# Kernel tuning notes

Hardware: AMD Instinct MI355X
Metric: run time of the kernel (lower is better)

The kernel has to match this reference:

```python
import jax, jax.numpy as jnp
import numpy as np

N = 50000      # nodes
E = 800000     # edges
H = 128        # hidden_features
EF = 8         # edge_features (before distance concat)
L = 2          # num_layers
NF = 100.0     # normalization_factor
NC = 1.0       # norm_constant
ATTN = True
USE_TANH = False
TANH_RANGE = 15.0
EIN = 2 * H + EF + 1  # GCL / coord-MLP edge input dim


def setup_inputs() -> dict:
    key = jax.random.key(0)
    ks = jax.random.split(key, 16)
    s = 0.02
    w = lambda k, shape: (jax.random.normal(k, shape, jnp.float32) * s)
    return dict(
        x=jax.random.normal(ks[0], (N, H), jnp.float32),
        pos=jax.random.normal(ks[1], (N, 3), jnp.float32),
        mask=jnp.ones((N, 1), jnp.float32),
        edge_attr=jax.random.normal(ks[2], (E, EF), jnp.float32),
        edge_index=jax.random.randint(ks[3], (2, E), 0, N),
        # GCL layer params, stacked over L layers
        W_e1=w(ks[4], (L, EIN, H)), b_e1=jnp.zeros((L, H), jnp.float32),
        W_e2=w(ks[5], (L, H, H)),  b_e2=jnp.zeros((L, H), jnp.float32),
        W_att=w(ks[6], (L, H, 1)), b_att=jnp.zeros((L, 1), jnp.float32),
        W_n1=w(ks[7], (L, 2 * H, H)), b_n1=jnp.zeros((L, H), jnp.float32),
        W_n2=w(ks[8], (L, H, H)),  b_n2=jnp.zeros((L, H), jnp.float32),
        # Equivariant coordinate-update MLP (last layer has no bias)
        cW1=w(ks[9], (EIN, H)), cb1=jnp.zeros((H,), jnp.float32),
        cW2=w(ks[10], (H, H)), cb2=jnp.zeros((H,), jnp.float32),
        cW3=w(ks[11], (H, 1)),
    )


def reference(x, pos, mask, edge_attr, edge_index,
              W_e1, b_e1, W_e2, b_e2, W_att, b_att, W_n1, b_n1, W_n2, b_n2,
              cW1, cb1, cW2, cb2, cW3):
    silu = jax.nn.silu
    row, col = edge_index[0], edge_index[1]  # aggregate messages at row
    diff = pos[row] - pos[col]                         # [E, 3]
    d2 = jnp.sum(diff * diff, axis=-1, keepdims=True)  # [E, 1] squared distance
    ea = jnp.concatenate([d2, edge_attr], axis=-1)     # [E, EF+1]

    # GCL message-passing layers (residual node update)
    for l in range(L):
        he = jnp.concatenate([x[row], x[col], ea], axis=-1)   # [E, EIN]
        m = silu(silu(he @ W_e1[l] + b_e1[l]) @ W_e2[l] + b_e2[l])
        if ATTN:
            m = m * jax.nn.sigmoid(m @ W_att[l] + b_att[l])
        agg = jax.ops.segment_sum(m, row, num_segments=N) / NF
        x = x + silu(jnp.concatenate([x, agg], axis=-1) @ W_n1[l] + b_n1[l]) @ W_n2[l] + b_n2[l]

    # Equivariant coordinate update
    he = jnp.concatenate([x[row], x[col], ea], axis=-1)
    phi = silu(silu(he @ cW1 + cb1) @ cW2 + cb2) @ cW3        # [E, 1]
    if USE_TANH:
        phi = jnp.tanh(phi) * TANH_RANGE
    nd = diff / (jnp.sqrt(d2) + NC)                           # normalized direction
    trans = nd * phi                                          # [E, 3]
    pos = pos + (jax.ops.segment_sum(trans, row, num_segments=N) / NF) * mask
    return (x, pos)
```

## Files before the change

### kernel.cpp

```cpp
#include <hip/hip_runtime.h>
#include <hip/hip_bf16.h>
#include <stdint.h>

#define NN 50000
#define NE 800000
#define HH 128

typedef __bf16 bf16x8 __attribute__((ext_vector_type(8)));
typedef float  f32x4  __attribute__((ext_vector_type(4)));
typedef long   f8frag;

__device__ __forceinline__ unsigned short f2bf(float f) {
  union { float f; uint32_t u; } v; v.f = f;
  uint32_t r = v.u + 0x7FFFu + ((v.u >> 16) & 1u);
  return (unsigned short)(r >> 16);
}
__device__ __forceinline__ float b2f(unsigned short u) {
  union { float f; uint32_t u; } v; v.u = (uint32_t)u << 16; return v.f;
}
#if __has_builtin(__builtin_amdgcn_cvt_pk_bf16_f32)
typedef __bf16 bf16x2 __attribute__((ext_vector_type(2)));
__device__ __forceinline__ uint32_t pack2bf(float a, float b) {
  union { bf16x2 v; uint32_t u; } t;
  t.v = __builtin_amdgcn_cvt_pk_bf16_f32(a, b);
  return t.u;
}
#else
__device__ __forceinline__ uint32_t pack2bf(float a, float b) {
  return (uint32_t)f2bf(a) | ((uint32_t)f2bf(b) << 16);
}
#endif
__device__ __forceinline__ uint8_t f2fp8(float v) {
  return (uint8_t)(__builtin_amdgcn_cvt_pk_fp8_f32(v, 0.f, 0, false) & 0xff);
}
__device__ __forceinline__ float silu_f(float x) {
  return x * __builtin_amdgcn_rcpf(1.f + __expf(-x));
}
__device__ __forceinline__ float sigm_f(float x) {
  return __builtin_amdgcn_rcpf(1.f + __expf(-x));
}

__device__ __forceinline__ bf16x8 frag_ld(const short* blk, int row, int q) {
  int c = q ^ ((row >> 1) & 3);
  return *(const bf16x8*)(blk + row * 32 + c * 8);
}
__device__ __forceinline__ int wfrag_off(int row, int q) {
  return row * 32 + ((q ^ ((row >> 1) & 3)) * 8);
}

__global__ void k_prep_weights(const float* We1, const float* We2, const float* Wn1,
                               const float* Wn2, const float* cW1, const float* cW2,
                               uint8_t* W1f8, short* W2sw, short* Wn1sw, short* Wn2sw,
                               short* W1csw) {
  int idx = blockIdx.x * 256 + threadIdx.x;
  if (idx < 110592) {
    int l = idx / 36864, rem = idx % 36864;
    const float* s = (l == 0) ? We1 : (l == 1) ? We1 + 33920 : cW1;
    int kkb = rem >> 12, r2 = rem & 4095;
    int n = r2 >> 5, kw = r2 & 31;
    int k = kkb * 32 + kw;
    float v = (k < 265) ? s[k * 128 + n] : 0.f;
    W1f8[idx] = f2fp8(v);
    return;
  }
  idx -= 110592;
  if (idx < 49152) {
    int l = idx >> 14, rem = idx & 16383;
    const float* s = (l == 0) ? We2 : (l == 1) ? We2 + 16384 : cW2;
    int kkb = rem >> 12, r2 = rem & 4095, n = r2 >> 5, kw = r2 & 31;
    int cp = kw >> 3, j = kw & 7, c = cp ^ ((n >> 1) & 3);
    int k = kkb * 32 + c * 8 + j;
    W2sw[(l << 14) + (rem)] = (short)f2bf(s[k * 128 + n]);
    return;
  }
  idx -= 49152;
  if (idx < 65536) {
    int l = idx >> 15, rem = idx & 32767;
    const float* s = Wn1 + l * 32768;
    int kkb = rem >> 12, r2 = rem & 4095, n = r2 >> 5, kw = r2 & 31;
    int cp = kw >> 3, j = kw & 7, c = cp ^ ((n >> 1) & 3);
    int k = kkb * 32 + c * 8 + j;
    Wn1sw[(l << 15) + rem] = (short)f2bf(s[k * 128 + n]);
    return;
  }
  idx -= 65536;
  if (idx < 32768) {
    int l = idx >> 14, rem = idx & 16383;
    const float* s = Wn2 + l * 16384;
    int kkb = rem >> 12, r2 = rem & 4095, n = r2 >> 5, kw = r2 & 31;
    int cp = kw >> 3, j = kw & 7, c = cp ^ ((n >> 1) & 3);
    int k = kkb * 32 + c * 8 + j;
    Wn2sw[(l << 14) + rem] = (short)f2bf(s[k * 128 + n]);
    return;
  }
  idx -= 32768;
  if (idx < 98304) {
    int l = idx / 32768, rem = idx % 32768;
    const float* s = (l == 0) ? We1 : (l == 1) ? We1 + 33920 : cW1;
    int kkb = rem >> 13, r2 = rem & 8191, n = r2 >> 5, kw = r2 & 31;
    int cp = kw >> 3, j = kw & 7, c = cp ^ ((n >> 1) & 3);
    int k = kkb * 32 + c * 8 + j;
    float v = (n < 128) ? s[k * 128 + n] : s[(128 + k) * 128 + (n - 128)];
    W1csw[l * 32768 + rem] = (short)f2bf(v);
  }
}

__global__ void k_x_prep(const float* __restrict__ x, short* __restrict__ Anode) {
  int i = blockIdx.x * 256 + threadIdx.x;
  if (i < NN * 32) {
    float4 v = ((const float4*)x)[i];
    ushort4 pk;
    pk.x = f2bf(v.x); pk.y = f2bf(v.y); pk.z = f2bf(v.z); pk.w = f2bf(v.w);
    *(ushort4*)(Anode + i * 4) = pk;
  }
}
__global__ void k_edge_pre(const float* __restrict__ pos, const float* __restrict__ eattr,
                           const int* __restrict__ ei, const int* __restrict__ inv,
                           int* __restrict__ rowS, int* __restrict__ colS,
                           uint8_t* __restrict__ eaF8, float* __restrict__ ndS) {
  int e = blockIdx.x * 256 + threadIdx.x;
  if (e >= NE) return;
  int r = ei[e], c = ei[NE + e];
  float dx = pos[r * 3 + 0] - pos[c * 3 + 0];
  float dy = pos[r * 3 + 1] - pos[c * 3 + 1];
  float dz = pos[r * 3 + 2] - pos[c * 3 + 2];
  float d2 = dx * dx + dy * dy + dz * dz;
  float invd = __builtin_amdgcn_rcpf(sqrtf(d2) + 1.f);
  int p = inv[e];
  rowS[p] = r;
  colS[p] = c;
  ndS[p * 3 + 0] = dx * invd;
  ndS[p * 3 + 1] = dy * invd;
  ndS[p * 3 + 2] = dz * invd;
  const float* ea = eattr + (size_t)e * 8;
  uint32_t w0 = __builtin_amdgcn_cvt_pk_fp8_f32(d2, ea[0], 0, false);
  w0 = __builtin_amdgcn_cvt_pk_fp8_f32(ea[1], ea[2], w0, true);
  uint32_t w1 = __builtin_amdgcn_cvt_pk_fp8_f32(ea[3], ea[4], 0, false);
  w1 = __builtin_amdgcn_cvt_pk_fp8_f32(ea[5], ea[6], w1, true);
  uint32_t w2 = __builtin_amdgcn_cvt_pk_fp8_f32(ea[7], 0.f, 0, false);
  uint4 v = {w0, w1, w2, 0u};
  *(uint4*)(eaF8 + (size_t)p * 16) = v;
}
__global__ void k_pos_final(const float* __restrict__ pos, const float* __restrict__ mask,
                            const float* __restrict__ pagg, float* __restrict__ out) {
  int i = blockIdx.x * 256 + threadIdx.x;
  if (i < NN * 3) out[i] = pos[i] + pagg[i] * 0.01f * mask[i / 3];
}

__global__ void k_hist(const int* __restrict__ ei, int* __restrict__ cnt) {
  int e = blockIdx.x * 256 + threadIdx.x;
  if (e < NE) atomicAdd(&cnt[ei[e]], 1);
}
__global__ void k_scan_block(const int* __restrict__ cnt, int* __restrict__ offs,
                             int* __restrict__ bsum) {
  __shared__ int s[256];
  int i = blockIdx.x * 256 + threadIdx.x;
  int v = (i < NN) ? cnt[i] : 0;
  s[threadIdx.x] = v;
  __syncthreads();
#pragma unroll
  for (int d = 1; d < 256; d <<= 1) {
    int t = (threadIdx.x >= d) ? s[threadIdx.x - d] : 0;
    __syncthreads();
    s[threadIdx.x] += t;
    __syncthreads();
  }
  if (i < NN) offs[i] = s[threadIdx.x] - v;
  if (threadIdx.x == 255) bsum[blockIdx.x] = s[255];
}
__global__ void k_scan_top(int* __restrict__ bsum) {
  __shared__ int s[256];
  int v = (threadIdx.x < 196) ? bsum[threadIdx.x] : 0;
  s[threadIdx.x] = v;
  __syncthreads();
#pragma unroll
  for (int d = 1; d < 256; d <<= 1) {
    int t = (threadIdx.x >= d) ? s[threadIdx.x - d] : 0;
    __syncthreads();
    s[threadIdx.x] += t;
    __syncthreads();
  }
  if (threadIdx.x < 196) bsum[threadIdx.x] = s[threadIdx.x] - v;
}
__global__ void k_scan_add(int* __restrict__ offs, const int* __restrict__ bsum) {
  int i = blockIdx.x * 256 + threadIdx.x;
  if (i < NN) offs[i] += bsum[blockIdx.x];
}
__global__ void k_scatter(const int* __restrict__ ei, int* __restrict__ offs,
                          int* __restrict__ inv) {
  int e = blockIdx.x * 256 + threadIdx.x;
  if (e < NE) inv[e] = atomicAdd(&offs[ei[e]], 1);
}

__global__ __launch_bounds__(256) void k_h1(
    const short* __restrict__ Anode, const short* __restrict__ W1c,
    const float* __restrict__ b1, short* __restrict__ H1RC) {
  const int tid = threadIdx.x, lane = tid & 63, w = tid >> 6;
  const int ln = lane & 15, q = lane >> 4;
  const int tile = blockIdx.x;
  size_t nbase[4];
  int wofs[4];
#pragma unroll
  for (int i = 0; i < 4; ++i) {
    int node = tile * 64 + i * 16 + ln;
    nbase[i] = (size_t)(node < NN ? node : (NN - 1)) * 128;
    int row = w * 64 + i * 16 + ln;
    wofs[i] = row * 32 + ((q ^ ((row >> 1) & 3)) * 8);
  }
  f32x4 acc[4][4];
  const f32x4 zero4 = {0.f, 0.f, 0.f, 0.f};
#pragma unroll
  for (int mi = 0; mi < 4; ++mi)
#pragma unroll
    for (int ni = 0; ni < 4; ++ni) acc[mi][ni] = zero4;
#pragma unroll
  for (int kk = 0; kk < 4; ++kk) {
    bf16x8 af[4], bfr[4];
#pragma unroll
    for (int i = 0; i < 4; ++i) af[i] = *(const bf16x8*)(Anode + nbase[i] + kk * 32 + q * 8);
#pragma unroll
    for (int i = 0; i < 4; ++i) bfr[i] = *(const bf16x8*)(W1c + kk * 8192 + wofs[i]);
#pragma unroll
    for (int mi = 0; mi < 4; ++mi)
#pragma unroll
      for (int ni = 0; ni < 4; ++ni)
        acc[mi][ni] = __builtin_amdgcn_mfma_f32_16x16x32_bf16(af[mi], bfr[ni], acc[mi][ni], 0, 0, 0);
  }
  float b1v[4];
#pragma unroll
  for (int ni = 0; ni < 4; ++ni) {
    int ch = w * 64 + ni * 16 + ln;
    b1v[ni] = (ch < 128) ? b1[ch] : 0.f;
  }
#pragma unroll
  for (int mi = 0; mi < 4; ++mi)
#pragma unroll
    for (int r = 0; r < 4; ++r) {
      int node = tile * 64 + mi * 16 + q * 4 + r;
      if (node < NN) {
#pragma unroll
        for (int ni = 0; ni < 4; ++ni) {
          int ph = (w >> 1) * 128 + (w & 1) * 64 + ((ln >> 2) << 4) + (ni << 2) + (ln & 3);
          H1RC[(size_t)node * 256 + ph] = (short)f2bf(acc[mi][ni][r] + b1v[ni]);
        }
      }
    }
}

template <int COORD>
__global__ __launch_bounds__(256, 4) void k_edge_gemm(
    const short* __restrict__ H1RC, const uint8_t* __restrict__ eaF8,
    const int* __restrict__ rowS, const int* __restrict__ colS,
    const uint8_t* __restrict__ W1f8, const short* __restrict__ W2l,
    const float* __restrict__ b2,
    const float* __restrict__ wred, const float* __restrict__ batt,
    const float* __restrict__ ndS, float* outAcc) {
  __shared__ __align__(16) short A2s[8192];
  __shared__ float redp[64][2];
  __shared__ __align__(16) unsigned short attb[64];
  __shared__ int srow[64];
  __shared__ __align__(8) unsigned char srunS[64];
  __shared__ int runrowS[64];
  __shared__ int cntS[1];

  const int tid = threadIdx.x;
  const int lane = tid & 63;
  const int w = tid >> 6;
  const int ln = lane & 15, q = lane >> 4;
  const int wm = w >> 1, wn = w & 1;
  const int tile = blockIdx.x;

  if (tid < 64) srow[tid] = rowS[tile * 64 + tid];
  __syncthreads();

  bool is_start = (tid < 64) && (tid == 0 || srow[tid] != srow[tid - 1]);
  unsigned long long bmask = __ballot(is_start);
  if (tid == 0) cntS[0] = __popcll(bmask);
  if (tid < 64) {
    int run = __popcll(bmask & ((1ull << lane) - 1ull)) + (is_start ? 1 : 0) - 1;
    srunS[tid] = (unsigned char)run;
    if (is_start) runrowS[run] = srow[tid];
  }

  const int e0 = wm * 32 + ln, e1 = e0 + 16;
  const uint32_t cbp = (uint32_t)(wn * 64 + q * 16);
  const uint32_t hr0 = (uint32_t)srow[e0] * 256u + cbp;
  const uint32_t hr1 = (uint32_t)srow[e1] * 256u + cbp;
  const uint32_t hc0 = (uint32_t)colS[tile * 64 + e0] * 256u + 128u + cbp;
  const uint32_t hc1 = (uint32_t)colS[tile * 64 + e1] * 256u + 128u + cbp;
  const uint32_t ea0 = (uint32_t)(tile * 64 + e0) * 16u + (uint32_t)((q & 1) * 8);
  const uint32_t ea1 = (uint32_t)(tile * 64 + e1) * 16u + (uint32_t)((q & 1) * 8);
  int wofs8[4], wofs[4];
#pragma unroll
  for (int i = 0; i < 4; ++i) {
    wofs8[i] = (wn * 64 + i * 16 + ln) * 32 + q * 8;
    wofs[i] = wfrag_off(wn * 64 + i * 16 + ln, q);
  }

  union U8 { uint4 v; unsigned short s[8]; };
  U8 xr[2][2], xc[2][2];
  xr[0][0].v = *(const uint4*)(H1RC + hr0);
  xr[0][1].v = *(const uint4*)(H1RC + hr0 + 8);
  xr[1][0].v = *(const uint4*)(H1RC + hr1);
  xr[1][1].v = *(const uint4*)(H1RC + hr1 + 8);
  xc[0][0].v = *(const uint4*)(H1RC + hc0);
  xc[0][1].v = *(const uint4*)(H1RC + hc0 + 8);
  xc[1][0].v = *(const uint4*)(H1RC + hc1);
  xc[1][1].v = *(const uint4*)(H1RC + hc1 + 8);

  f32x4 acc[4][2];
  const f32x4 zero4 = {0.f, 0.f, 0.f, 0.f};
#pragma unroll
  for (int ni = 0; ni < 4; ++ni)
#pragma unroll
    for (int mi = 0; mi < 2; ++mi) acc[ni][mi] = zero4;

  {
    const uint8_t* W1ea = W1f8 + 8 * 4096;
    f8frag wf[4], hf[2];
#pragma unroll
    for (int i = 0; i < 4; ++i) wf[i] = *(const f8frag*)(W1ea + wofs8[i]);
    hf[0] = (q < 2) ? *(const f8frag*)(eaF8 + ea0) : 0L;
    hf[1] = (q < 2) ? *(const f8frag*)(eaF8 + ea1) : 0L;
#pragma unroll
    for (int ni = 0; ni < 4; ++ni)
#pragma unroll
      for (int mi = 0; mi < 2; ++mi)
        acc[ni][mi] = __builtin_amdgcn_mfma_f32_16x16x32_fp8_fp8(wf[ni], hf[mi], acc[ni][mi], 0, 0, 0);
  }

#pragma unroll
  for (int ni = 0; ni < 4; ++ni) {
    int cb = wn * 64 + ni * 16 + q * 4;
    int kkb = cb >> 5, cc = (cb >> 3) & 3, j0 = cb & 7;
    const int hh = ni >> 1, b4 = (ni & 1) * 4;
#pragma unroll
    for (int mi = 0; mi < 2; ++mi) {
      int edge = wm * 32 + mi * 16 + ln;
      int addr = kkb * 2048 + edge * 32 + ((cc ^ ((edge >> 1) & 3)) * 8) + j0;
      float h0 = silu_f(acc[ni][mi][0] + b2f(xr[mi][hh].s[b4 + 0]) + b2f(xc[mi][hh].s[b4 + 0]));
      float h1 = silu_f(acc[ni][mi][1] + b2f(xr[mi][hh].s[b4 + 1]) + b2f(xc[mi][hh].s[b4 + 1]));
      float h2 = silu_f(acc[ni][mi][2] + b2f(xr[mi][hh].s[b4 + 2]) + b2f(xc[mi][hh].s[b4 + 2]));
      float h3 = silu_f(acc[ni][mi][3] + b2f(xr[mi][hh].s[b4 + 3]) + b2f(xc[mi][hh].s[b4 + 3]));
      uint2 pk;
      pk.x = pack2bf(h0, h1);
      pk.y = pack2bf(h2, h3);
      *(uint2*)(A2s + addr) = pk;
    }
  }
  __syncthreads();

  f32x4 acc2[4][2];
#pragma unroll
  for (int ni = 0; ni < 4; ++ni)
#pragma unroll
    for (int mi = 0; mi < 2; ++mi) acc2[ni][mi] = zero4;
#pragma unroll
  for (int kk = 0; kk < 4; ++kk) {
    bf16x8 wf[4], hf[2];
#pragma unroll
    for (int i = 0; i < 4; ++i) wf[i] = *(const bf16x8*)(W2l + kk * 4096 + wofs[i]);
#pragma unroll
    for (int i = 0; i < 2; ++i) hf[i] = frag_ld(A2s + kk * 2048, wm * 32 + i * 16 + ln, q);
#pragma unroll
    for (int ni = 0; ni < 4; ++ni)
#pragma unroll
      for (int mi = 0; mi < 2; ++mi)
        acc2[ni][mi] = __builtin_amdgcn_mfma_f32_16x16x32_bf16(wf[ni], hf[mi], acc2[ni][mi], 0, 0, 0);
  }

  float4 b2v[4], wv[4];
#pragma unroll
  for (int ni = 0; ni < 4; ++ni) {
    b2v[ni] = *(const float4*)(b2 + wn * 64 + ni * 16 + q * 4);
    wv[ni]  = *(const float4*)(wred + wn * 64 + ni * 16 + q * 4);
  }
  float p[2] = {0.f, 0.f};
#pragma unroll
  for (int ni = 0; ni < 4; ++ni)
#pragma unroll
    for (int mi = 0; mi < 2; ++mi)
#pragma unroll
      for (int r = 0; r < 4; ++r) {
        float v = silu_f(acc2[ni][mi][r] + ((const float*)&b2v[ni])[r]);
        acc2[ni][mi][r] = v;
        p[mi] += v * ((const float*)&wv[ni])[r];
      }
#pragma unroll
  for (int mi = 0; mi < 2; ++mi) {
    p[mi] += __shfl_xor(p[mi], 16, 64);
    p[mi] += __shfl_xor(p[mi], 32, 64);
  }
  if (lane < 16) {
#pragma unroll
    for (int mi = 0; mi < 2; ++mi) redp[wm * 32 + mi * 16 + ln][wn] = p[mi];
  }
  __syncthreads();

  if (COORD == 0) {
    if (tid < 64) attb[tid] = f2bf(sigm_f(redp[tid][0] + redp[tid][1] + batt[0]));
#pragma unroll
    for (int ni = 0; ni < 4; ++ni)
#pragma unroll
      for (int mi = 0; mi < 2; ++mi) {
        int eb = mi * 16 + ln;
        int cE = (eb >> 3) & 3, jE = eb & 7;
#pragma unroll
        for (int r = 0; r < 4; ++r) {
          int chan2 = wn * 64 + ni * 16 + q * 4 + r;
          int addr = wm * 4096 + chan2 * 32 + ((cE ^ ((chan2 >> 1) & 3)) * 8) + jE;
          union { float f; uint32_t u; } vv;
          vv.f = acc2[ni][mi][r];
          A2s[addr] = (short)((vv.u + 0x8000u) >> 16);
        }
      }
    __syncthreads();
    const int nruns = cntS[0];
    bf16x8 bfrg[2][2];
#pragma unroll
    for (int kk = 0; kk < 2; ++kk)
#pragma unroll
      for (int ni = 0; ni < 2; ++ni)
        bfrg[kk][ni] = frag_ld(A2s + kk * 4096, w * 32 + ni * 16 + ln, q);
    const int npass = (nruns + 15) >> 4;
    for (int pp = 0; pp < npass; ++pp) {
      const unsigned int base = pp * 16;
      f32x4 a3c[2] = {zero4, zero4};
#pragma unroll
      for (int kk = 0; kk < 2; ++kk) {
        uint2 sb = *(const uint2*)(srunS + kk * 32 + q * 8);
        U8 ab;
        ab.v = *(const uint4*)(attb + kk * 32 + q * 8);
        union { short s[8]; bf16x8 v; } af;
#pragma unroll
        for (int j = 0; j < 4; ++j)
          af.s[j] = (((sb.x >> (8 * j)) & 255u) == base + (unsigned)ln) ? (short)ab.s[j] : (short)0;
#pragma unroll
        for (int j = 0; j < 4; ++j)
          af.s[4 + j] = (((sb.y >> (8 * j)) & 255u) == base + (unsigned)ln) ? (short)ab.s[4 + j] : (short)0;
        a3c[0] = __builtin_amdgcn_mfma_f32_16x16x32_bf16(af.v, bfrg[kk][0], a3c[0], 0, 0, 0);
        a3c[1] = __builtin_amdgcn_mfma_f32_16x16x32_bf16(af.v, bfrg[kk][1], a3c[1], 0, 0, 0);
      }
#pragma unroll
      for (int ni = 0; ni < 2; ++ni)
#pragma unroll
        for (int r = 0; r < 4; ++r) {
          int run = (int)base + q * 4 + r;
          if (run < nruns) {
            int rw = runrowS[run];
            atomicAdd(&outAcc[(size_t)rw * 128 + (w * 32 + ni * 16 + ln)], a3c[ni][r]);
          }
        }
    }
  } else {
    float* ndl = (float*)A2s;
    if (tid < 64) {
      float phi = redp[tid][0] + redp[tid][1];
      ndl[tid * 3 + 0] = ndS[(size_t)(tile * 64 + tid) * 3 + 0] * phi;
      ndl[tid * 3 + 1] = ndS[(size_t)(tile * 64 + tid) * 3 + 1] * phi;
      ndl[tid * 3 + 2] = ndS[(size_t)(tile * 64 + tid) * 3 + 2] * phi;
    }
    __syncthreads();
    if (is_start) {
      int myrow = srow[tid];
      float s0 = 0.f, s1 = 0.f, s2 = 0.f;
      for (int j = tid; j < 64 && srow[j] == myrow; ++j) {
        s0 += ndl[j * 3 + 0];
        s1 += ndl[j * 3 + 1];
        s2 += ndl[j * 3 + 2];
      }
      atomicAdd(&outAcc[myrow * 3 + 0], s0);
      atomicAdd(&outAcc[myrow * 3 + 1], s1);
      atomicAdd(&outAcc[myrow * 3 + 2], s2);
    }
  }
}

__global__ __launch_bounds__(256) void k_node_gemm(
    short* Anode, const float* __restrict__ agg,
    const short* __restrict__ Wn1l, const short* __restrict__ Wn2l,
    const float* __restrict__ b1, const float* __restrict__ b2,
    const float* __restrict__ xres, float* __restrict__ xout) {
  __shared__ short A2s[4 * 2048];

  const int tid = threadIdx.x;
  const int lane = tid & 63;
  const int w = tid >> 6;
  const int ln = lane & 15, q = lane >> 4;
  const int wm = w >> 1, wn = w & 1;
  const int tile = blockIdx.x;

  int nidx[2];
  size_t nbase[2];
  int wofs[4];
#pragma unroll
  for (int i = 0; i < 2; ++i) {
    int node = tile * 64 + wm * 32 + i * 16 + ln;
    nidx[i] = node < NN ? node : (NN - 1);
    nbase[i] = (size_t)nidx[i] * 128;
  }
#pragma unroll
  for (int i = 0; i < 4; ++i) wofs[i] = wfrag_off(wn * 64 + i * 16 + ln, q);

  f32x4 acc[2][4];
  const f32x4 zero4 = {0.f, 0.f, 0.f, 0.f};
#pragma unroll
  for (int mi = 0; mi < 2; ++mi)
#pragma unroll
    for (int ni = 0; ni < 4; ++ni) acc[mi][ni] = zero4;

#pragma unroll
  for (int kk = 0; kk < 8; ++kk) {
    bf16x8 af[2], bfr[4];
#pragma unroll
    for (int i = 0; i < 2; ++i) {
      if (kk < 4) {
        af[i] = *(const bf16x8*)(Anode + nbase[i] + kk * 32 + q * 8);
      } else {
        const float* ag = agg + nbase[i] + (kk - 4) * 32 + q * 8;
        float4 lo = *(const float4*)ag;
        float4 hi = *(const float4*)(ag + 4);
        union { uint32_t u[4]; bf16x8 v; } t;
        t.u[0] = pack2bf(lo.x * 0.01f, lo.y * 0.01f);
        t.u[1] = pack2bf(lo.z * 0.01f, lo.w * 0.01f);
        t.u[2] = pack2bf(hi.x * 0.01f, hi.y * 0.01f);
        t.u[3] = pack2bf(hi.z * 0.01f, hi.w * 0.01f);
        af[i] = t.v;
      }
    }
#pragma unroll
    for (int i = 0; i < 4; ++i) bfr[i] = *(const bf16x8*)(Wn1l + kk * 4096 + wofs[i]);
#pragma unroll
    for (int mi = 0; mi < 2; ++mi)
#pragma unroll
      for (int ni = 0; ni < 4; ++ni)
        acc[mi][ni] = __builtin_amdgcn_mfma_f32_16x16x32_bf16(af[mi], bfr[ni], acc[mi][ni], 0, 0, 0);
  }

  float b1v[4];
#pragma unroll
  for (int ni = 0; ni < 4; ++ni) b1v[ni] = b1[wn * 64 + ni * 16 + ln];
#pragma unroll
  for (int mi = 0; mi < 2; ++mi)
#pragma unroll
    for (int ni = 0; ni < 4; ++ni) {
      int chan = wn * 64 + ni * 16 + ln;
      int kkb = chan >> 5, c = (chan >> 3) & 3, jj = chan & 7;
#pragma unroll
      for (int r = 0; r < 4; ++r) {
        int m = wm * 32 + mi * 16 + q * 4 + r;
        float v = silu_f(acc[mi][ni][r] + b1v[ni]);
        A2s[kkb * 2048 + m * 32 + ((c ^ ((m >> 1) & 3)) * 8) + jj] = (short)f2bf(v);
      }
    }
  __syncthreads();

  f32x4 acc2[2][4];
#pragma unroll
  for (int mi = 0; mi < 2; ++mi)
#pragma unroll
    for (int ni = 0; ni < 4; ++ni) acc2[mi][ni] = zero4;
#pragma unroll
  for (int kk = 0; kk < 4; ++kk) {
    bf16x8 af[2], bfr[4];
#pragma unroll
    for (int i = 0; i < 2; ++i) af[i] = frag_ld(A2s + kk * 2048, wm * 32 + i * 16 + ln, q);
#pragma unroll
    for (int i = 0; i < 4; ++i) bfr[i] = *(const bf16x8*)(Wn2l + kk * 4096 + wofs[i]);
#pragma unroll
    for (int mi = 0; mi < 2; ++mi)
#pragma unroll
      for (int ni = 0; ni < 4; ++ni)
        acc2[mi][ni] = __builtin_amdgcn_mfma_f32_16x16x32_bf16(af[mi], bfr[ni], acc2[mi][ni], 0, 0, 0);
  }

  float b2v[4];
#pragma unroll
  for (int ni = 0; ni < 4; ++ni) b2v[ni] = b2[wn * 64 + ni * 16 + ln];
#pragma unroll
  for (int mi = 0; mi < 2; ++mi)
#pragma unroll
    for (int r = 0; r < 4; ++r) {
      int m = wm * 32 + mi * 16 + q * 4 + r;
      int node = tile * 64 + m;
      if (node < NN) {
#pragma unroll
        for (int ni = 0; ni < 4; ++ni) {
          int chan = wn * 64 + ni * 16 + ln;
          float v = acc2[mi][ni][r] + b2v[ni] + xres[(size_t)node * 128 + chan];
          xout[(size_t)node * 128 + chan] = v;
          Anode[(size_t)node * 128 + chan] = (short)f2bf(v);
        }
      }
    }
}

extern "C" void kernel_launch(void* const* d_in, const int* in_sizes, int n_in,
                              void* d_out, int out_size, void* d_ws, size_t ws_size,
                              hipStream_t stream) {
  const float* x    = (const float*)d_in[0];
  const float* pos  = (const float*)d_in[1];
  const float* mask = (const float*)d_in[2];
  const float* eattr= (const float*)d_in[3];
  const int*   ei   = (const int*)d_in[4];
  const float* We1  = (const float*)d_in[5];
  const float* be1  = (const float*)d_in[6];
  const float* We2  = (const float*)d_in[7];
  const float* be2  = (const float*)d_in[8];
  const float* Watt = (const float*)d_in[9];
  const float* batt = (const float*)d_in[10];
  const float* Wn1  = (const float*)d_in[11];
  const float* bn1  = (const float*)d_in[12];
  const float* Wn2  = (const float*)d_in[13];
  const float* bn2  = (const float*)d_in[14];
  const float* cW1  = (const float*)d_in[15];
  const float* cb1  = (const float*)d_in[16];
  const float* cW2  = (const float*)d_in[17];
  const float* cb2  = (const float*)d_in[18];
  const float* cW3  = (const float*)d_in[19];

  char* p = (char*)d_ws;
  auto carve = [&](size_t bytes) { char* r = p; p += (bytes + 511) & ~(size_t)511; return r; };
  short*   Anode = (short*)carve((size_t)NN * 128 * 2);
  short*   H1RC  = (short*)carve((size_t)NN * 256 * 2);
  uint8_t* eaF8  = (uint8_t*)carve((size_t)NE * 16 + 256);
  int*     rowS  = (int*)carve((size_t)NE * 4);
  int*     colS  = (int*)carve((size_t)NE * 4);
  float*   ndS   = (float*)carve((size_t)NE * 3 * 4);
  float*   agg   = (float*)carve((size_t)NN * 128 * 4);
  float*   xcur  = (float*)carve((size_t)NN * 128 * 4);
  float*   pagg  = (float*)carve((size_t)NN * 3 * 4);
  uint8_t* W1f8  = (uint8_t*)carve(3 * 36864);
  short*   W2sw  = (short*)carve(3 * 16384 * 2);
  short*   Wn1sw = (short*)carve(2 * 32768 * 2);
  short*   Wn2sw = (short*)carve(2 * 16384 * 2);
  short*   W1csw = (short*)carve(3 * 32768 * 2);
  int*     cnt   = (int*)carve((size_t)NN * 4);
  int*     offs  = (int*)carve((size_t)NN * 4);
  int*     bsum  = (int*)carve(256 * 4);
  int*     inv   = (int*)carve((size_t)NE * 4);

  float* xout_f = (float*)d_out;
  float* pout_f = xout_f + NN * 128;

  k_prep_weights<<<1392, 256, 0, stream>>>(We1, We2, Wn1, Wn2, cW1, cW2,
                                           W1f8, W2sw, Wn1sw, Wn2sw, W1csw);
  k_x_prep<<<6250, 256, 0, stream>>>(x, Anode);

  hipMemsetAsync(cnt, 0, (size_t)NN * 4, stream);
  k_hist<<<3125, 256, 0, stream>>>(ei, cnt);
  k_scan_block<<<196, 256, 0, stream>>>(cnt, offs, bsum);
  k_scan_top<<<1, 256, 0, stream>>>(bsum);
  k_scan_add<<<196, 256, 0, stream>>>(offs, bsum);
  k_scatter<<<3125, 256, 0, stream>>>(ei, offs, inv);
  k_edge_pre<<<3125, 256, 0, stream>>>(pos, eattr, ei, inv, rowS, colS, eaF8, ndS);

  for (int l = 0; l < 2; ++l) {
    k_h1<<<782, 256, 0, stream>>>(Anode, W1csw + l * 32768, be1 + l * 128, H1RC);
    hipMemsetAsync(agg, 0, (size_t)NN * 128 * 4, stream);
    k_edge_gemm<0><<<12500, 256, 0, stream>>>(H1RC, eaF8, rowS, colS,
        W1f8 + l * 36864, W2sw + l * 16384, be2 + l * 128,
        Watt + l * 128, batt + l, (const float*)nullptr, agg);
    k_node_gemm<<<782, 256, 0, stream>>>(Anode, agg,
        Wn1sw + l * 32768, Wn2sw + l * 16384, bn1 + l * 128, bn2 + l * 128,
        l == 0 ? x : xcur, l == 0 ? xcur : xout_f);
  }
  k_h1<<<782, 256, 0, stream>>>(Anode, W1csw + 2 * 32768, cb1, H1RC);
  hipMemsetAsync(pagg, 0, (size_t)NN * 3 * 4, stream);
  k_edge_gemm<1><<<12500, 256, 0, stream>>>(H1RC, eaF8, rowS, colS,
      W1f8 + 2 * 36864, W2sw + 2 * 16384, cb2, cW3, (const float*)nullptr, ndS, pagg);
  k_pos_final<<<587, 256, 0, stream>>>(pos, mask, pagg, pout_f);
}
```

Before: 720.5 us.

## Fuse next-layer H1 projection into node GEMM and drop bf16 node copy

After: 712.2 us. No clear change (-1.2%).

```diff
diff --git a/kernel.cpp b/kernel.cpp
--- a/kernel.cpp
+++ b/kernel.cpp
@@ -46,6 +46,16 @@
 }
 __device__ __forceinline__ int wfrag_off(int row, int q) {
   return row * 32 + ((q ^ ((row >> 1) & 3)) * 8);
+}
+__device__ __forceinline__ bf16x8 fragf32(const float* src, float sc) {
+  float4 lo = *(const float4*)src;
+  float4 hi = *(const float4*)(src + 4);
+  union { uint32_t u[4]; bf16x8 v; } t;
+  t.u[0] = pack2bf(lo.x * sc, lo.y * sc);
+  t.u[1] = pack2bf(lo.z * sc, lo.w * sc);
+  t.u[2] = pack2bf(hi.x * sc, hi.y * sc);
+  t.u[3] = pack2bf(hi.z * sc, hi.w * sc);
+  return t.v;
 }
 
 __global__ void k_prep_weights(const float* We1, const float* We2, const float* Wn1,
@@ -105,15 +115,6 @@
   }
 }
 
-__global__ void k_x_prep(const float* __restrict__ x, short* __restrict__ Anode) {
-  int i = blockIdx.x * 256 + threadIdx.x;
-  if (i < NN * 32) {
-    float4 v = ((const float4*)x)[i];
-    ushort4 pk;
-    pk.x = f2bf(v.x); pk.y = f2bf(v.y); pk.z = f2bf(v.z); pk.w = f2bf(v.w);
-    *(ushort4*)(Anode + i * 4) = pk;
-  }
-}
 __global__ void k_edge_pre(const float* __restrict__ pos, const float* __restrict__ eattr,
                            const int* __restrict__ ei, const int* __restrict__ inv,
                            int* __restrict__ rowS, int* __restrict__ colS,
@@ -193,7 +194,7 @@
 }
 
 __global__ __launch_bounds__(256) void k_h1(
-    const short* __restrict__ Anode, const short* __restrict__ W1c,
+    const float* __restrict__ x, const short* __restrict__ W1c,
     const float* __restrict__ b1, short* __restrict__ H1RC) {
   const int tid = threadIdx.x, lane = tid & 63, w = tid >> 6;
   const int ln = lane & 15, q = lane >> 4;
@@ -217,7 +218,7 @@
   for (int kk = 0; kk < 4; ++kk) {
     bf16x8 af[4], bfr[4];
 #pragma unroll
-    for (int i = 0; i < 4; ++i) af[i] = *(const bf16x8*)(Anode + nbase[i] + kk * 32 + q * 8);
+    for (int i = 0; i < 4; ++i) af[i] = fragf32(x + nbase[i] + kk * 32 + q * 8, 1.f);
 #pragma unroll
     for (int i = 0; i < 4; ++i) bfr[i] = *(const bf16x8*)(W1c + kk * 8192 + wofs[i]);
 #pragma unroll
@@ -238,11 +239,12 @@
     for (int r = 0; r < 4; ++r) {
       int node = tile * 64 + mi * 16 + q * 4 + r;
       if (node < NN) {
-#pragma unroll
-        for (int ni = 0; ni < 4; ++ni) {
-          int ph = (w >> 1) * 128 + (w & 1) * 64 + ((ln >> 2) << 4) + (ni << 2) + (ln & 3);
-          H1RC[(size_t)node * 256 + ph] = (short)f2bf(acc[mi][ni][r] + b1v[ni]);
-        }
+        ushort4 pk;
+        pk.x = f2bf(acc[mi][0][r] + b1v[0]);
+        pk.y = f2bf(acc[mi][1][r] + b1v[1]);
+        pk.z = f2bf(acc[mi][2][r] + b1v[2]);
+        pk.w = f2bf(acc[mi][3][r] + b1v[3]);
+        *(ushort4*)(H1RC + (size_t)node * 256 + w * 64 + ln * 4) = pk;
       }
     }
 }
@@ -268,7 +270,11 @@
   const int w = tid >> 6;
   const int ln = lane & 15, q = lane >> 4;
   const int wm = w >> 1, wn = w & 1;
-  const int tile = blockIdx.x;
+
+  const int nwg = gridDim.x;
+  const int qq = nwg >> 3, rr = nwg & 7;
+  const int xcd = blockIdx.x & 7, bidx = blockIdx.x >> 3;
+  const int tile = (xcd < rr ? xcd * (qq + 1) : rr * (qq + 1) + (xcd - rr) * qq) + bidx;
 
   if (tid < 64) srow[tid] = rowS[tile * 64 + tid];
   __syncthreads();
@@ -333,15 +339,14 @@
   for (int ni = 0; ni < 4; ++ni) {
     int cb = wn * 64 + ni * 16 + q * 4;
     int kkb = cb >> 5, cc = (cb >> 3) & 3, j0 = cb & 7;
-    const int hh = ni >> 1, b4 = (ni & 1) * 4;
 #pragma unroll
     for (int mi = 0; mi < 2; ++mi) {
       int edge = wm * 32 + mi * 16 + ln;
       int addr = kkb * 2048 + edge * 32 + ((cc ^ ((edge >> 1) & 3)) * 8) + j0;
-      float h0 = silu_f(acc[ni][mi][0] + b2f(xr[mi][hh].s[b4 + 0]) + b2f(xc[mi][hh].s[b4 + 0]));
-      float h1 = silu_f(acc[ni][mi][1] + b2f(xr[mi][hh].s[b4 + 1]) + b2f(xc[mi][hh].s[b4 + 1]));
-      float h2 = silu_f(acc[ni][mi][2] + b2f(xr[mi][hh].s[b4 + 2]) + b2f(xc[mi][hh].s[b4 + 2]));
-      float h3 = silu_f(acc[ni][mi][3] + b2f(xr[mi][hh].s[b4 + 3]) + b2f(xc[mi][hh].s[b4 + 3]));
+      float h0 = silu_f(acc[ni][mi][0] + b2f(xr[mi][0].s[ni]) + b2f(xc[mi][0].s[ni]));
+      float h1 = silu_f(acc[ni][mi][1] + b2f(xr[mi][0].s[4 + ni]) + b2f(xc[mi][0].s[4 + ni]));
+      float h2 = silu_f(acc[ni][mi][2] + b2f(xr[mi][1].s[ni]) + b2f(xc[mi][1].s[ni]));
+      float h3 = silu_f(acc[ni][mi][3] + b2f(xr[mi][1].s[4 + ni]) + b2f(xc[mi][1].s[4 + ni]));
       uint2 pk;
       pk.x = pack2bf(h0, h1);
       pk.y = pack2bf(h2, h3);
@@ -477,10 +482,12 @@
 }
 
 __global__ __launch_bounds__(256) void k_node_gemm(
-    short* Anode, const float* __restrict__ agg,
+    const float* __restrict__ agg,
     const short* __restrict__ Wn1l, const short* __restrict__ Wn2l,
     const float* __restrict__ b1, const float* __restrict__ b2,
-    const float* __restrict__ xres, float* __restrict__ xout) {
+    const float* __restrict__ xres, float* __restrict__ xout,
+    const short* __restrict__ W1cN, const float* __restrict__ b1N,
+    short* __restrict__ H1RC) {
   __shared__ short A2s[4 * 2048];
 
   const int tid = threadIdx.x;
@@ -490,14 +497,12 @@
   const int wm = w >> 1, wn = w & 1;
   const int tile = blockIdx.x;
 
-  int nidx[2];
   size_t nbase[2];
   int wofs[4];
 #pragma unroll
   for (int i = 0; i < 2; ++i) {
     int node = tile * 64 + wm * 32 + i * 16 + ln;
-    nidx[i] = node < NN ? node : (NN - 1);
-    nbase[i] = (size_t)nidx[i] * 128;
+    nbase[i] = (size_t)(node < NN ? node : (NN - 1)) * 128;
   }
 #pragma unroll
   for (int i = 0; i < 4; ++i) wofs[i] = wfrag_off(wn * 64 + i * 16 + ln, q);
@@ -514,19 +519,8 @@
     bf16x8 af[2], bfr[4];
 #pragma unroll
     for (int i = 0; i < 2; ++i) {
-      if (kk < 4) {
-        af[i] = *(const bf16x8*)(Anode + nbase[i] + kk * 32 + q * 8);
-      } else {
-        const float* ag = agg + nbase[i] + (kk - 4) * 32 + q * 8;
-        float4 lo = *(const float4*)ag;
-        float4 hi = *(const float4*)(ag + 4);
-        union { uint32_t u[4]; bf16x8 v; } t;
-        t.u[0] = pack2bf(lo.x * 0.01f, lo.y * 0.01f);
-        t.u[1] = pack2bf(lo.z * 0.01f, lo.w * 0.01f);
-        t.u[2] = pack2bf(hi.x * 0.01f, hi.y * 0.01f);
-        t.u[3] = pack2bf(hi.z * 0.01f, hi.w * 0.01f);
-        af[i] = t.v;
-      }
+      if (kk < 4) af[i] = fragf32(xres + nbase[i] + kk * 32 + q * 8, 1.f);
+      else        af[i] = fragf32(agg + nbase[i] + (kk - 4) * 32 + q * 8, 0.01f);
     }
 #pragma unroll
     for (int i = 0; i < 4; ++i) bfr[i] = *(const bf16x8*)(Wn1l + kk * 4096 + wofs[i]);
@@ -588,9 +582,69 @@
         for (int ni = 0; ni < 4; ++ni) {
           int chan = wn * 64 + ni * 16 + ln;
           float v = acc2[mi][ni][r] + b2v[ni] + xres[(size_t)node * 128 + chan];
+          acc2[mi][ni][r] = v;
           xout[(size_t)node * 128 + chan] = v;
-          Anode[(size_t)node * 128 + chan] = (short)f2bf(v);
         }
+      }
+    }
+
+  __syncthreads();
+#pragma unroll
+  for (int mi = 0; mi < 2; ++mi)
+#pragma unroll
+    for (int ni = 0; ni < 4; ++ni) {
+      int chan = wn * 64 + ni * 16 + ln;
+      int kkb = chan >> 5, c = (chan >> 3) & 3, jj = chan & 7;
+#pragma unroll
+      for (int r = 0; r < 4; ++r) {
+        int m = wm * 32 + mi * 16 + q * 4 + r;
+        A2s[kkb * 2048 + m * 32 + ((c ^ ((m >> 1) & 3)) * 8) + jj] = (short)f2bf(acc2[mi][ni][r]);
+      }
+    }
+  __syncthreads();
+
+  int wofsH[4];
+#pragma unroll
+  for (int i = 0; i < 4; ++i) {
+    int row = w * 64 + i * 16 + ln;
+    wofsH[i] = row * 32 + ((q ^ ((row >> 1) & 3)) * 8);
+  }
+  f32x4 acc3[4][4];
+#pragma unroll
+  for (int mi = 0; mi < 4; ++mi)
+#pragma unroll
+    for (int ni = 0; ni < 4; ++ni) acc3[mi][ni] = zero4;
+#pragma unroll
+  for (int kk = 0; kk < 4; ++kk) {
+    bf16x8 af[4], bfr[4];
+#pragma unroll
+    for (int i = 0; i < 4; ++i) af[i] = frag_ld(A2s + kk * 2048, i * 16 + ln, q);
+#pragma unroll
+    for (int i = 0; i < 4; ++i) bfr[i] = *(const bf16x8*)(W1cN + kk * 8192 + wofsH[i]);
+#pragma unroll
+    for (int mi = 0; mi < 4; ++mi)
+#pragma unroll
+      for (int ni = 0; ni < 4; ++ni)
+        acc3[mi][ni] = __builtin_amdgcn_mfma_f32_16x16x32_bf16(af[mi], bfr[ni], acc3[mi][ni], 0, 0, 0);
+  }
+  float b1v2[4];
+#pragma unroll
+  for (int ni = 0; ni < 4; ++ni) {
+    int ch = w * 64 + ni * 16 + ln;
+    b1v2[ni] = (ch < 128) ? b1N[ch] : 0.f;
+  }
+#pragma unroll
+  for (int mi = 0; mi < 4; ++mi)
+#pragma unroll
+    for (int r = 0; r < 4; ++r) {
+      int node = tile * 64 + mi * 16 + q * 4 + r;
+      if (node < NN) {
+        ushort4 pk;
+        pk.x = f2bf(acc3[mi][0][r] + b1v2[0]);
+        pk.y = f2bf(acc3[mi][1][r] + b1v2[1]);
+        pk.z = f2bf(acc3[mi][2][r] + b1v2[2]);
+        pk.w = f2bf(acc3[mi][3][r] + b1v2[3]);
+        *(ushort4*)(H1RC + (size_t)node * 256 + w * 64 + ln * 4) = pk;
       }
     }
 }
@@ -621,7 +675,6 @@
 
   char* p = (char*)d_ws;
   auto carve = [&](size_t bytes) { char* r = p; p += (bytes + 511) & ~(size_t)511; return r; };
-  short*   Anode = (short*)carve((size_t)NN * 128 * 2);
   short*   H1RC  = (short*)carve((size_t)NN * 256 * 2);
   uint8_t* eaF8  = (uint8_t*)carve((size_t)NE * 16 + 256);
   int*     rowS  = (int*)carve((size_t)NE * 4);
@@ -645,7 +698,6 @@
 
   k_prep_weights<<<1392, 256, 0, stream>>>(We1, We2, Wn1, Wn2, cW1, cW2,
                                            W1f8, W2sw, Wn1sw, Wn2sw, W1csw);
-  k_x_prep<<<6250, 256, 0, stream>>>(x, Anode);
 
   hipMemsetAsync(cnt, 0, (size_t)NN * 4, stream);
   k_hist<<<3125, 256, 0, stream>>>(ei, cnt);
@@ -655,17 +707,21 @@
   k_scatter<<<3125, 256, 0, stream>>>(ei, offs, inv);
   k_edge_pre<<<3125, 256, 0, stream>>>(pos, eattr, ei, inv, rowS, colS, eaF8, ndS);
 
-  for (int l = 0; l < 2; ++l) {
-    k_h1<<<782, 256, 0, stream>>>(Anode, W1csw + l * 32768, be1 + l * 128, H1RC);
-    hipMemsetAsync(agg, 0, (size_t)NN * 128 * 4, stream);
-    k_edge_gemm<0><<<12500, 256, 0, stream>>>(H1RC, eaF8, rowS, colS,
-        W1f8 + l * 36864, W2sw + l * 16384, be2 + l * 128,
-        Watt + l * 128, batt + l, (const float*)nullptr, agg);
-    k_node_gemm<<<782, 256, 0, stream>>>(Anode, agg,
-        Wn1sw + l * 32768, Wn2sw + l * 16384, bn1 + l * 128, bn2 + l * 128,
-        l == 0 ? x : xcur, l == 0 ? xcur : xout_f);
-  }
-  k_h1<<<782, 256, 0, stream>>>(Anode, W1csw + 2 * 32768, cb1, H1RC);
+  k_h1<<<782, 256, 0, stream>>>(x, W1csw, be1, H1RC);
+
+  hipMemsetAsync(agg, 0, (size_t)NN * 128 * 4, stream);
+  k_edge_gemm<0><<<12500, 256, 0, stream>>>(H1RC, eaF8, rowS, colS,
+      W1f8, W2sw, be2, Watt, batt, (const float*)nullptr, agg);
+  k_node_gemm<<<782, 256, 0, stream>>>(agg, Wn1sw, Wn2sw, bn1, bn2,
+      x, xcur, W1csw + 32768, be1 + 128, H1RC);
+
+  hipMemsetAsync(agg, 0, (size_t)NN * 128 * 4, stream);
+  k_edge_gemm<0><<<12500, 256, 0, stream>>>(H1RC, eaF8, rowS, colS,
+      W1f8 + 36864, W2sw + 16384, be2 + 128, Watt + 128, batt + 1,
+      (const float*)nullptr, agg);
+  k_node_gemm<<<782, 256, 0, stream>>>(agg, Wn1sw + 32768, Wn2sw + 16384,
+      bn1 + 128, bn2 + 128, xcur, xout_f, W1csw + 2 * 32768, cb1, H1RC);
+
   hipMemsetAsync(pagg, 0, (size_t)NN * 3 * 4, stream);
   k_edge_gemm<1><<<12500, 256, 0, stream>>>(H1RC, eaF8, rowS, colS,
       W1f8 + 2 * 36864, W2sw + 2 * 16384, cb2, cW3, (const float*)nullptr, ndS, pagg);
```
